# Kernel optimization log

Hardware: AMD Instinct MI355X
Metric: run time of the kernel (lower is better)

## Reference

```python
import jax, jax.numpy as jnp
import numpy as np

B, Z, A = 1024, 512, 8          # batch_size, z_dim, action_dim
AH, ZH = 64, 512                # action_hidden_dim, z_hidden_dim
N_NEG = 100                     # n_neg_actions
TEMP = 0.1                      # temperature
TOP_K = (1, 3, 10)


def forward_model(z, a, Wa, ba, W1, b1, W2, b2):
    # MLP forward model with skip connection (z_delta=True):
    # embed action, concat with z, 2-layer MLP predicting a delta.
    h_a = jax.nn.relu(a @ Wa + ba)                                   # [..., AH]
    h = jax.nn.relu(jnp.concatenate([jnp.broadcast_to(z, a.shape[:-1] + (Z,)), h_a], axis=-1) @ W1 + b1)  # [..., ZH]
    delta = h @ W2 + b2                                              # [..., Z]
    return z + delta


def setup_inputs() -> dict:
    key = jax.random.key(0)
    ks = jax.random.split(key, 8)
    def w(k, shape, fan_in):
        return jax.random.normal(k, shape, jnp.float32) / np.float32(np.sqrt(fan_in))
    z = jax.random.normal(ks[0], (B, Z), jnp.float32)
    z_next = jax.random.normal(ks[1], (B, Z), jnp.float32)
    z_next_hat = jax.random.normal(ks[2], (B, Z), jnp.float32)
    actions = jax.random.normal(ks[3], (B, A), jnp.float32)
    Wa = w(ks[4], (A, AH), A)
    ba = jnp.zeros((AH,), jnp.float32)
    W1 = w(ks[5], (Z + AH, ZH), Z + AH)
    b1 = jnp.zeros((ZH,), jnp.float32)
    W2 = w(ks[6], (ZH, Z), ZH)
    b2 = jnp.zeros((Z,), jnp.float32)
    return {"z": z, "z_next": z_next, "z_next_hat": z_next_hat, "actions": actions,
            "Wa": Wa, "ba": ba, "W1": W1, "b1": b1, "W2": W2, "b2": b2}


def reference(z, z_next, z_next_hat, actions, Wa, ba, W1, b1, W2, b2):
    # ControlCPC.compute_loss with dot_product_similarity, vectorized:
    # the Python loop over n_neg_actions rolled-action forward-model calls
    # becomes one batched [n-1, B, ...] forward-model evaluation.
    batch = z.shape[0]
    n = min(N_NEG, batch)
    sim = z_next @ z_next_hat.T                                      # [B, B] positives on diagonal
    shifts = jnp.arange(1, n)
    neg_actions = jax.vmap(lambda i: jnp.roll(actions, -i, axis=0))(shifts)  # [n-1, B, A]
    z_hat_neg = forward_model(z[None], neg_actions, Wa, ba, W1, b1, W2, b2)  # [n-1, B, Z]
    neg_sim = jnp.einsum('nbz,bz->bn', z_hat_neg, z_next)            # diag of similarity per shift
    sim_mat = jnp.concatenate([sim, neg_sim], axis=1)                # [B, B+n-1]
    # INCE loss, positives on diagonal
    logp = jax.nn.log_softmax(sim_mat / jnp.float32(TEMP), axis=1)
    loss = -jnp.mean(jnp.diagonal(logp))                             # diagonal takes first B entries
    labels = jnp.arange(batch)[:, None]
    accs = []
    for k in TOP_K:
        _, preds = jax.lax.top_k(sim_mat, k)                         # [B, k]
        accs.append(jnp.mean((preds == labels).astype(jnp.float32)) * k)
    return (loss, accs[0], accs[1], accs[2])
```

## Files before the change

kernel.cpp:

```cpp
#include <hip/hip_runtime.h>
#include <math.h>

#define B_SZ 1024
#define Z_DIM 512
#define A_DIM 8
#define AH 64
#define ZH 512
#define NNEG 99
#define ROWLEN (B_SZ + NNEG)
#define INV_T 10.0f

typedef __attribute__((ext_vector_type(8))) short short8;
typedef __attribute__((ext_vector_type(4))) float f32x4;

__device__ __forceinline__ void cvt_hilo(float4 x0, float4 x1, short8& hi, short8& lo) {
    float xs[8] = {x0.x, x0.y, x0.z, x0.w, x1.x, x1.y, x1.z, x1.w};
#pragma unroll
    for (int i = 0; i < 8; ++i) {
        unsigned u = __float_as_uint(xs[i]);
        hi[i] = (short)(u >> 16);
        float hf = __uint_as_float(u & 0xffff0000u);
        float lf = xs[i] - hf;
        lo[i] = (short)(__float_as_uint(lf) >> 16);
    }
}

__global__ __launch_bounds__(256) void fused_gemm(
    const float* __restrict__ z, const float* __restrict__ z_next,
    const float* __restrict__ z_next_hat, const float* __restrict__ actions,
    const float* __restrict__ Wa, const float* __restrict__ ba,
    const float* __restrict__ W1, const float* __restrict__ b1,
    const float* __restrict__ W2,
    float* __restrict__ sim, float* __restrict__ u, float* __restrict__ v,
    float* __restrict__ g, unsigned* __restrict__ cnt)
{
    __shared__ float LA[64][68];
    __shared__ float LB[64][68];
    __shared__ float sact[64][A_DIM];
    __shared__ float sWa[A_DIM * AH];
    __shared__ float sba[AH];

    const int id = blockIdx.x;
    const int tid = threadIdx.x;
    if (id == 0 && tid == 0) *cnt = 0;

    if (id >= 512) {
        int t = id - 512;
        int bn0 = (t & 7) * 64, bm0 = (t >> 3) * 64;
        const float* W1h = W1 + Z_DIM * ZH;
        for (int i = tid; i < 64 * A_DIM; i += 256)
            (&sact[0][0])[i] = actions[bm0 * A_DIM + i];
        for (int i = tid; i < A_DIM * AH; i += 256) sWa[i] = Wa[i];
        if (tid < AH) sba[tid] = ba[tid];
        __syncthreads();
        int tm = (tid >> 4) << 2, tn = (tid & 15) << 2;
        float acc[4][4] = {};
        for (int k0 = 0; k0 < 64; k0 += 32) {
#pragma unroll
            for (int i = 0; i < 8; ++i) {
                int lin = tid + i * 256;
                int c = lin & 31, r = lin >> 5;
                int kc = k0 + c;
                float val = sba[kc];
#pragma unroll
                for (int k = 0; k < A_DIM; ++k) val += sact[r][k] * sWa[k * AH + kc];
                LA[c][r] = fmaxf(val, 0.0f);
            }
#pragma unroll
            for (int i = 0; i < 2; ++i) {
                int f = tid + i * 256;
                int r = f >> 4, c = (f & 15) * 4;
                *(float4*)&LB[r][c] = *(const float4*)&W1h[(k0 + r) * ZH + bn0 + c];
            }
            __syncthreads();
#pragma unroll
            for (int k = 0; k < 32; ++k) {
                float4 a4 = *(const float4*)&LA[k][tm];
                float4 b4 = *(const float4*)&LB[k][tn];
                float a[4] = {a4.x, a4.y, a4.z, a4.w};
                float b[4] = {b4.x, b4.y, b4.z, b4.w};
#pragma unroll
                for (int i = 0; i < 4; ++i)
#pragma unroll
                    for (int j = 0; j < 4; ++j) acc[i][j] += a[i] * b[j];
            }
            __syncthreads();
        }
#pragma unroll
        for (int i = 0; i < 4; ++i) {
            float4 o = {acc[i][0], acc[i][1], acc[i][2], acc[i][3]};
            *(float4*)&g[(bm0 + tm + i) * ZH + bn0 + tn] = o;
        }
        return;
    }

    const float* Aop; const float* Bop; const float* bias = nullptr;
    float* C; int N; bool btrans; int bm0, bn0;
    if (id < 256) {
        int t = id; bn0 = (t & 15) * 64; bm0 = (t >> 4) * 64;
        Aop = z_next; Bop = z_next_hat; C = sim; N = 1024; btrans = true;
    } else if (id < 384) {
        int t = id - 256; bn0 = (t & 7) * 64; bm0 = (t >> 3) * 64;
        Aop = z; Bop = W1; C = u; N = 512; btrans = false; bias = b1;
    } else {
        int t = id - 384; bn0 = (t & 7) * 64; bm0 = (t >> 3) * 64;
        Aop = z_next; Bop = W2; C = v; N = 512; btrans = true;
    }

    const int lane = tid & 63, wv = tid >> 6;
    const int lm = lane & 15, lq = lane >> 4;
    const int wm = (wv >> 1) * 32, wn = (wv & 1) * 32;
    f32x4 acc[2][2] = {};

    for (int k0 = 0; k0 < 512; k0 += 64) {
#pragma unroll
        for (int i = 0; i < 4; ++i) {
            int gg = tid + i * 256;
            int r = gg >> 4, c4 = (gg & 15) << 2;
            *(float4*)&LA[r][c4] = *(const float4*)&Aop[(bm0 + r) * 512 + k0 + c4];
        }
        if (btrans) {
#pragma unroll
            for (int i = 0; i < 4; ++i) {
                int gg = tid + i * 256;
                int r = gg >> 4, c4 = (gg & 15) << 2;
                *(float4*)&LB[r][c4] = *(const float4*)&Bop[(bn0 + r) * 512 + k0 + c4];
            }
        } else {
#pragma unroll
            for (int i = 0; i < 4; ++i) {
                int gg = tid + i * 256;
                int kr = gg >> 4, n4 = (gg & 15) << 2;
                float4 w = *(const float4*)&Bop[(k0 + kr) * 512 + bn0 + n4];
                LB[n4 + 0][kr] = w.x; LB[n4 + 1][kr] = w.y;
                LB[n4 + 2][kr] = w.z; LB[n4 + 3][kr] = w.w;
            }
        }
        __syncthreads();
#pragma unroll
        for (int kk = 0; kk < 64; kk += 32) {
            int kb = kk + lq * 8;
            short8 ah[2], al[2], bh[2], bl[2];
#pragma unroll
            for (int i = 0; i < 2; ++i) {
                float4 x0 = *(const float4*)&LA[wm + i * 16 + lm][kb];
                float4 x1 = *(const float4*)&LA[wm + i * 16 + lm][kb + 4];
                cvt_hilo(x0, x1, ah[i], al[i]);
                float4 y0 = *(const float4*)&LB[wn + i * 16 + lm][kb];
                float4 y1 = *(const float4*)&LB[wn + i * 16 + lm][kb + 4];
                cvt_hilo(y0, y1, bh[i], bl[i]);
            }
#pragma unroll
            for (int i = 0; i < 2; ++i)
#pragma unroll
                for (int j = 0; j < 2; ++j) {
                    acc[i][j] = __builtin_amdgcn_mfma_f32_16x16x32_bf16(ah[i], bh[j], acc[i][j], 0, 0, 0);
                    acc[i][j] = __builtin_amdgcn_mfma_f32_16x16x32_bf16(ah[i], bl[j], acc[i][j], 0, 0, 0);
                    acc[i][j] = __builtin_amdgcn_mfma_f32_16x16x32_bf16(al[i], bh[j], acc[i][j], 0, 0, 0);
                }
        }
        __syncthreads();
    }
#pragma unroll
    for (int i = 0; i < 2; ++i)
#pragma unroll
        for (int j = 0; j < 2; ++j) {
            int n = bn0 + wn + j * 16 + lm;
            float bb = bias ? bias[n] : 0.0f;
#pragma unroll
            for (int r = 0; r < 4; ++r) {
                int m = bm0 + wm + i * 16 + lq * 4 + r;
                C[m * N + n] = acc[i][j][r] + bb;
            }
        }
}

__global__ __launch_bounds__(256) void row_kernel(const float* __restrict__ sim,
                                                  const float* __restrict__ u,
                                                  const float* __restrict__ v,
                                                  const float* __restrict__ g,
                                                  const float* __restrict__ z,
                                                  const float* __restrict__ z_next,
                                                  const float* __restrict__ b2,
                                                  float* __restrict__ pw,
                                                  unsigned* __restrict__ cnt,
                                                  float* __restrict__ out) {
    int b = blockIdx.x;
    int tid = threadIdx.x;
    int wave = tid >> 6, lane = tid & 63;
    __shared__ float su[ZH];
    __shared__ float sv[ZH];
    __shared__ float row[ROWLEN];
    __shared__ float redc0[4], redmax[4], redes[4];
    __shared__ int redcnt[4];
    __shared__ float red[256];
    __shared__ int sdone;

    {
        const float4* u4 = (const float4*)(u + b * ZH);
        const float4* v4 = (const float4*)(v + b * ZH);
        if (tid < ZH / 4) {
            *(float4*)&su[tid * 4] = u4[tid];
            *(float4*)&sv[tid * 4] = v4[tid];
        }
        const float4* s4 = (const float4*)(sim + b * B_SZ);
        *(float4*)&row[tid * 4] = s4[tid];
    }
    float p = 0.0f;
    {
        const float4* z4 = (const float4*)(z + b * Z_DIM);
        const float4* zn4 = (const float4*)(z_next + b * Z_DIM);
        const float4* b24 = (const float4*)b2;
        if (tid < Z_DIM / 4) {
            float4 a = z4[tid], c = b24[tid], n = zn4[tid];
            p = (a.x + c.x) * n.x + (a.y + c.y) * n.y + (a.z + c.z) * n.z + (a.w + c.w) * n.w;
        }
    }
    for (int off = 32; off; off >>= 1) p += __shfl_down(p, off);
    if (lane == 0) redc0[wave] = p;
    __syncthreads();

    float c0 = redc0[0] + redc0[1] + redc0[2] + redc0[3];

    for (int s = 1 + wave; s <= NNEG; s += 4) {
        int jr = (b + s) & (B_SZ - 1);
        const float4* gr4 = (const float4*)(g + jr * ZH);
        float d = 0.0f;
#pragma unroll
        for (int i = 0; i < 2; ++i) {
            int t4 = lane + i * 64;
            float4 gv = gr4[t4];
            float4 uv = *(const float4*)&su[t4 * 4];
            float4 vv = *(const float4*)&sv[t4 * 4];
            d += fmaxf(uv.x + gv.x, 0.0f) * vv.x;
            d += fmaxf(uv.y + gv.y, 0.0f) * vv.y;
            d += fmaxf(uv.z + gv.z, 0.0f) * vv.z;
            d += fmaxf(uv.w + gv.w, 0.0f) * vv.w;
        }
        for (int off = 32; off; off >>= 1) d += __shfl_down(d, off);
        if (lane == 0) row[B_SZ + s - 1] = c0 + d;
    }
    __syncthreads();

    float diag = row[b];
    float m = -3.4e38f;
    for (int j = tid; j < ROWLEN; j += 256) m = fmaxf(m, row[j]);
    for (int off = 32; off; off >>= 1) m = fmaxf(m, __shfl_down(m, off));
    if (lane == 0) redmax[wave] = m;
    __syncthreads();
    m = fmaxf(fmaxf(redmax[0], redmax[1]), fmaxf(redmax[2], redmax[3]));

    float es = 0.0f;
    int cntk = 0;
    for (int j = tid; j < ROWLEN; j += 256) {
        float x = row[j];
        es += __expf((x - m) * INV_T);
        if (x > diag) cntk++;
        else if (j < b && x == diag) cntk++;
    }
    for (int off = 32; off; off >>= 1) {
        es += __shfl_down(es, off);
        cntk += __shfl_down(cntk, off);
    }
    __syncthreads();
    if (lane == 0) { redes[wave] = es; redcnt[wave] = cntk; }
    __syncthreads();
    if (tid == 0) {
        float esum = redes[0] + redes[1] + redes[2] + redes[3];
        int rank = redcnt[0] + redcnt[1] + redcnt[2] + redcnt[3];
        float loss_b = (m - diag) * INV_T + logf(esum);
        pw[b * 4 + 0] = loss_b;
        pw[b * 4 + 1] = (rank < 1) ? 1.0f : 0.0f;
        pw[b * 4 + 2] = (rank < 3) ? 1.0f : 0.0f;
        pw[b * 4 + 3] = (rank < 10) ? 1.0f : 0.0f;
        __threadfence();
        unsigned old = atomicAdd(cnt, 1u);
        sdone = (old == B_SZ - 1) ? 1 : 0;
    }
    __syncthreads();
    if (sdone) {
        __threadfence();
        int c = tid & 3;
        float s = 0.0f;
        for (int r = tid >> 2; r < B_SZ; r += 64) s += pw[r * 4 + c];
        red[tid] = s;
        __syncthreads();
        if (tid < 4) {
            float t = 0.0f;
            for (int gg = 0; gg < 64; ++gg) t += red[tid + gg * 4];
            out[tid] = t * (1.0f / (float)B_SZ);
        }
    }
}

extern "C" void kernel_launch(void* const* d_in, const int* in_sizes, int n_in,
                              void* d_out, int out_size, void* d_ws, size_t ws_size,
                              hipStream_t stream) {
    const float* z          = (const float*)d_in[0];
    const float* z_next     = (const float*)d_in[1];
    const float* z_next_hat = (const float*)d_in[2];
    const float* actions    = (const float*)d_in[3];
    const float* Wa         = (const float*)d_in[4];
    const float* ba         = (const float*)d_in[5];
    const float* W1         = (const float*)d_in[6];
    const float* b1         = (const float*)d_in[7];
    const float* W2         = (const float*)d_in[8];
    const float* b2         = (const float*)d_in[9];
    float* out = (float*)d_out;

    float* ws  = (float*)d_ws;
    float* sim = ws;
    float* u   = sim + B_SZ * B_SZ;
    float* v   = u + B_SZ * ZH;
    float* g   = v + B_SZ * ZH;
    float* pw  = g + B_SZ * ZH;
    unsigned* cnt = (unsigned*)(pw + B_SZ * 4);

    fused_gemm<<<640, 256, 0, stream>>>(z, z_next, z_next_hat, actions, Wa, ba,
                                        W1, b1, W2, sim, u, v, g, cnt);
    row_kernel<<<B_SZ, 256, 0, stream>>>(sim, u, v, g, z, z_next, b2, pw, cnt, out);
}
```

Measured before the change: 134.0 us.

## Pre-split bf16 hi/lo in LDS and batch neg-shift loads in row kernel

The MFMA GEMM path now converts fp32 tiles to bf16 hi/lo pairs once while staging into shared memory, using a union with the fp32 segment's buffers. This removes the repeated per-wave conversion work and halves the LDS read width per operand. The row kernel keeps u/v in registers instead of shared memory and processes four negative shifts per iteration, with batched g loads and interleaved shuffle reductions for more memory-level parallelism. The transposed short stores into LDS may cause bank conflicts, and register pressure rises.

```diff
diff --git a/kernel.cpp b/kernel.cpp
--- a/kernel.cpp
+++ b/kernel.cpp
@@ -11,19 +11,25 @@
 #define INV_T 10.0f
 
 typedef __attribute__((ext_vector_type(8))) short short8;
+typedef __attribute__((ext_vector_type(4))) short short4_t;
 typedef __attribute__((ext_vector_type(4))) float f32x4;
 
-__device__ __forceinline__ void cvt_hilo(float4 x0, float4 x1, short8& hi, short8& lo) {
-    float xs[8] = {x0.x, x0.y, x0.z, x0.w, x1.x, x1.y, x1.z, x1.w};
-#pragma unroll
-    for (int i = 0; i < 8; ++i) {
-        unsigned u = __float_as_uint(xs[i]);
-        hi[i] = (short)(u >> 16);
-        float hf = __uint_as_float(u & 0xffff0000u);
-        float lf = xs[i] - hf;
-        lo[i] = (short)(__float_as_uint(lf) >> 16);
+__device__ __forceinline__ void cvt4(float4 x, short4_t& hi, short4_t& lo) {
+    float xs[4] = {x.x, x.y, x.z, x.w};
+#pragma unroll
+    for (int i = 0; i < 4; ++i) {
+        unsigned uu = __float_as_uint(xs[i]);
+        hi[i] = (short)(uu >> 16);
+        float hf = __uint_as_float(uu & 0xffff0000u);
+        lo[i] = (short)(__float_as_uint(xs[i] - hf) >> 16);
     }
 }
+
+struct MfmaSmem { short Ah[64][72]; short Al[64][72]; short Bh[64][72]; short Bl[64][72]; };
+struct Seg3Smem {
+    float LA[32][68]; float LB[32][68];
+    float sact[64][A_DIM]; float sWa[A_DIM * AH]; float sba[AH];
+};
 
 __global__ __launch_bounds__(256) void fused_gemm(
     const float* __restrict__ z, const float* __restrict__ z_next,
@@ -34,11 +40,7 @@
     float* __restrict__ sim, float* __restrict__ u, float* __restrict__ v,
     float* __restrict__ g, unsigned* __restrict__ cnt)
 {
-    __shared__ float LA[64][68];
-    __shared__ float LB[64][68];
-    __shared__ float sact[64][A_DIM];
-    __shared__ float sWa[A_DIM * AH];
-    __shared__ float sba[AH];
+    __shared__ union { MfmaSmem m; Seg3Smem s; } sm;
 
     const int id = blockIdx.x;
     const int tid = threadIdx.x;
@@ -49,9 +51,9 @@
         int bn0 = (t & 7) * 64, bm0 = (t >> 3) * 64;
         const float* W1h = W1 + Z_DIM * ZH;
         for (int i = tid; i < 64 * A_DIM; i += 256)
-            (&sact[0][0])[i] = actions[bm0 * A_DIM + i];
-        for (int i = tid; i < A_DIM * AH; i += 256) sWa[i] = Wa[i];
-        if (tid < AH) sba[tid] = ba[tid];
+            (&sm.s.sact[0][0])[i] = actions[bm0 * A_DIM + i];
+        for (int i = tid; i < A_DIM * AH; i += 256) sm.s.sWa[i] = Wa[i];
+        if (tid < AH) sm.s.sba[tid] = ba[tid];
         __syncthreads();
         int tm = (tid >> 4) << 2, tn = (tid & 15) << 2;
         float acc[4][4] = {};
@@ -61,22 +63,22 @@
                 int lin = tid + i * 256;
                 int c = lin & 31, r = lin >> 5;
                 int kc = k0 + c;
-                float val = sba[kc];
-#pragma unroll
-                for (int k = 0; k < A_DIM; ++k) val += sact[r][k] * sWa[k * AH + kc];
-                LA[c][r] = fmaxf(val, 0.0f);
+                float val = sm.s.sba[kc];
+#pragma unroll
+                for (int k = 0; k < A_DIM; ++k) val += sm.s.sact[r][k] * sm.s.sWa[k * AH + kc];
+                sm.s.LA[c][r] = fmaxf(val, 0.0f);
             }
 #pragma unroll
             for (int i = 0; i < 2; ++i) {
                 int f = tid + i * 256;
                 int r = f >> 4, c = (f & 15) * 4;
-                *(float4*)&LB[r][c] = *(const float4*)&W1h[(k0 + r) * ZH + bn0 + c];
+                *(float4*)&sm.s.LB[r][c] = *(const float4*)&W1h[(k0 + r) * ZH + bn0 + c];
             }
             __syncthreads();
 #pragma unroll
             for (int k = 0; k < 32; ++k) {
-                float4 a4 = *(const float4*)&LA[k][tm];
-                float4 b4 = *(const float4*)&LB[k][tn];
+                float4 a4 = *(const float4*)&sm.s.LA[k][tm];
+                float4 b4 = *(const float4*)&sm.s.LB[k][tn];
                 float a[4] = {a4.x, a4.y, a4.z, a4.w};
                 float b[4] = {b4.x, b4.y, b4.z, b4.w};
 #pragma unroll
@@ -117,14 +119,20 @@
         for (int i = 0; i < 4; ++i) {
             int gg = tid + i * 256;
             int r = gg >> 4, c4 = (gg & 15) << 2;
-            *(float4*)&LA[r][c4] = *(const float4*)&Aop[(bm0 + r) * 512 + k0 + c4];
+            float4 av = *(const float4*)&Aop[(bm0 + r) * 512 + k0 + c4];
+            short4_t hi, lo; cvt4(av, hi, lo);
+            *(short4_t*)&sm.m.Ah[r][c4] = hi;
+            *(short4_t*)&sm.m.Al[r][c4] = lo;
         }
         if (btrans) {
 #pragma unroll
             for (int i = 0; i < 4; ++i) {
                 int gg = tid + i * 256;
                 int r = gg >> 4, c4 = (gg & 15) << 2;
-                *(float4*)&LB[r][c4] = *(const float4*)&Bop[(bn0 + r) * 512 + k0 + c4];
+                float4 bv = *(const float4*)&Bop[(bn0 + r) * 512 + k0 + c4];
+                short4_t hi, lo; cvt4(bv, hi, lo);
+                *(short4_t*)&sm.m.Bh[r][c4] = hi;
+                *(short4_t*)&sm.m.Bl[r][c4] = lo;
             }
         } else {
 #pragma unroll
@@ -132,8 +140,12 @@
                 int gg = tid + i * 256;
                 int kr = gg >> 4, n4 = (gg & 15) << 2;
                 float4 w = *(const float4*)&Bop[(k0 + kr) * 512 + bn0 + n4];
-                LB[n4 + 0][kr] = w.x; LB[n4 + 1][kr] = w.y;
-                LB[n4 + 2][kr] = w.z; LB[n4 + 3][kr] = w.w;
+                short4_t hi, lo; cvt4(w, hi, lo);
+#pragma unroll
+                for (int e = 0; e < 4; ++e) {
+                    sm.m.Bh[n4 + e][kr] = hi[e];
+                    sm.m.Bl[n4 + e][kr] = lo[e];
+                }
             }
         }
         __syncthreads();
@@ -143,12 +155,10 @@
             short8 ah[2], al[2], bh[2], bl[2];
 #pragma unroll
             for (int i = 0; i < 2; ++i) {
-                float4 x0 = *(const float4*)&LA[wm + i * 16 + lm][kb];
-                float4 x1 = *(const float4*)&LA[wm + i * 16 + lm][kb + 4];
-                cvt_hilo(x0, x1, ah[i], al[i]);
-                float4 y0 = *(const float4*)&LB[wn + i * 16 + lm][kb];
-                float4 y1 = *(const float4*)&LB[wn + i * 16 + lm][kb + 4];
-                cvt_hilo(y0, y1, bh[i], bl[i]);
+                ah[i] = *(const short8*)&sm.m.Ah[wm + i * 16 + lm][kb];
+                al[i] = *(const short8*)&sm.m.Al[wm + i * 16 + lm][kb];
+                bh[i] = *(const short8*)&sm.m.Bh[wn + i * 16 + lm][kb];
+                bl[i] = *(const short8*)&sm.m.Bl[wn + i * 16 + lm][kb];
             }
 #pragma unroll
             for (int i = 0; i < 2; ++i)
@@ -188,57 +198,70 @@
     int b = blockIdx.x;
     int tid = threadIdx.x;
     int wave = tid >> 6, lane = tid & 63;
-    __shared__ float su[ZH];
-    __shared__ float sv[ZH];
     __shared__ float row[ROWLEN];
     __shared__ float redc0[4], redmax[4], redes[4];
     __shared__ int redcnt[4];
     __shared__ float red[256];
     __shared__ int sdone;
 
-    {
-        const float4* u4 = (const float4*)(u + b * ZH);
-        const float4* v4 = (const float4*)(v + b * ZH);
-        if (tid < ZH / 4) {
-            *(float4*)&su[tid * 4] = u4[tid];
-            *(float4*)&sv[tid * 4] = v4[tid];
-        }
-        const float4* s4 = (const float4*)(sim + b * B_SZ);
-        *(float4*)&row[tid * 4] = s4[tid];
-    }
+    *(float4*)&row[tid * 4] = ((const float4*)(sim + b * B_SZ))[tid];
+
+    const float4* u4 = (const float4*)(u + b * ZH);
+    const float4* v4 = (const float4*)(v + b * ZH);
+    float4 uva = u4[lane], uvb = u4[lane + 64];
+    float4 vva = v4[lane], vvb = v4[lane + 64];
+
     float p = 0.0f;
-    {
+    if (tid < 128) {
         const float4* z4 = (const float4*)(z + b * Z_DIM);
         const float4* zn4 = (const float4*)(z_next + b * Z_DIM);
         const float4* b24 = (const float4*)b2;
-        if (tid < Z_DIM / 4) {
-            float4 a = z4[tid], c = b24[tid], n = zn4[tid];
-            p = (a.x + c.x) * n.x + (a.y + c.y) * n.y + (a.z + c.z) * n.z + (a.w + c.w) * n.w;
-        }
+        float4 a = z4[tid], c = b24[tid], n = zn4[tid];
+        p = (a.x + c.x) * n.x + (a.y + c.y) * n.y + (a.z + c.z) * n.z + (a.w + c.w) * n.w;
     }
     for (int off = 32; off; off >>= 1) p += __shfl_down(p, off);
     if (lane == 0) redc0[wave] = p;
     __syncthreads();
-
     float c0 = redc0[0] + redc0[1] + redc0[2] + redc0[3];
 
-    for (int s = 1 + wave; s <= NNEG; s += 4) {
-        int jr = (b + s) & (B_SZ - 1);
-        const float4* gr4 = (const float4*)(g + jr * ZH);
-        float d = 0.0f;
-#pragma unroll
-        for (int i = 0; i < 2; ++i) {
-            int t4 = lane + i * 64;
-            float4 gv = gr4[t4];
-            float4 uv = *(const float4*)&su[t4 * 4];
-            float4 vv = *(const float4*)&sv[t4 * 4];
-            d += fmaxf(uv.x + gv.x, 0.0f) * vv.x;
-            d += fmaxf(uv.y + gv.y, 0.0f) * vv.y;
-            d += fmaxf(uv.z + gv.z, 0.0f) * vv.z;
-            d += fmaxf(uv.w + gv.w, 0.0f) * vv.w;
-        }
-        for (int off = 32; off; off >>= 1) d += __shfl_down(d, off);
-        if (lane == 0) row[B_SZ + s - 1] = c0 + d;
+    const float4* g4 = (const float4*)g;
+    int nIter = (wave < 3) ? 25 : 24;
+    for (int i0 = 0; i0 < nIter; i0 += 4) {
+        int nact = nIter - i0; if (nact > 4) nact = 4;
+        float4 ga[4], gb[4];
+        int ss[4];
+#pragma unroll
+        for (int j = 0; j < 4; ++j) {
+            int s = 1 + wave + 4 * (i0 + j);
+            ss[j] = s;
+            int se = (j < nact) ? s : 1;
+            int jr = (b + se) & (B_SZ - 1);
+            ga[j] = g4[jr * 128 + lane];
+            gb[j] = g4[jr * 128 + 64 + lane];
+        }
+        float d[4];
+#pragma unroll
+        for (int j = 0; j < 4; ++j) {
+            float t = 0.0f;
+            t += fmaxf(uva.x + ga[j].x, 0.0f) * vva.x;
+            t += fmaxf(uva.y + ga[j].y, 0.0f) * vva.y;
+            t += fmaxf(uva.z + ga[j].z, 0.0f) * vva.z;
+            t += fmaxf(uva.w + ga[j].w, 0.0f) * vva.w;
+            t += fmaxf(uvb.x + gb[j].x, 0.0f) * vvb.x;
+            t += fmaxf(uvb.y + gb[j].y, 0.0f) * vvb.y;
+            t += fmaxf(uvb.z + gb[j].z, 0.0f) * vvb.z;
+            t += fmaxf(uvb.w + gb[j].w, 0.0f) * vvb.w;
+            d[j] = t;
+        }
+        for (int off = 32; off; off >>= 1) {
+#pragma unroll
+            for (int j = 0; j < 4; ++j) d[j] += __shfl_down(d[j], off);
+        }
+        if (lane == 0) {
+#pragma unroll
+            for (int j = 0; j < 4; ++j)
+                if (j < nact) row[B_SZ + ss[j] - 1] = c0 + d[j];
+        }
     }
     __syncthreads();
 
```

After: 157.7 us. 1.18x slower.
